# Kernel tuning notes

Measured on AMD Instinct MI355X. Metric: run time of the kernel, lower is better.

The kernel has to match this reference:

```python
import jax, jax.numpy as jnp
import numpy as np

B, N, DIM, HEADS = 4, 1024, 1024, 16
DH = DIM // HEADS
SCALE = 1.0 / np.sqrt(DH)
EPS = 1e-6


def clinear(x, Wr, Wi, br, bi):
    # (a+bi)(Wr+Wi i): real = a Wr^T - b Wi^T, imag = a Wi^T + b Wr^T
    xr, xi = x.real, x.imag
    real = xr @ Wr.T - xi @ Wi.T + br
    imag = xr @ Wi.T + xi @ Wr.T + bi
    return jax.lax.complex(real, imag)


def cln(x, gamma, beta):
    # normalize magnitude over last dim, keep phase
    mag = jnp.abs(x)
    phase = jnp.angle(x)
    mean = jnp.mean(mag, axis=-1, keepdims=True)
    var = jnp.var(mag, axis=-1, keepdims=True)
    nm = (mag - mean) / jnp.sqrt(var + EPS)
    nm = nm * gamma + beta
    return jax.lax.complex(nm * jnp.cos(phase), nm * jnp.sin(phase))


def forward(xr, xi, Wq_r, Wq_i, bq_r, bq_i, Wk_r, Wk_i, bk_r, bk_i,
            Wv_r, Wv_i, bv_r, bv_i, Wo_r, Wo_i, bo_r, bo_i,
            gq, beq, gk, bek, gv, bev):
    x = jax.lax.complex(xr, xi)  # [B,N,D] complex64

    def heads(t):
        return t.reshape(B, N, HEADS, DH).transpose(0, 2, 1, 3)  # [B,H,N,dh]

    Q = heads(cln(clinear(x, Wq_r, Wq_i, bq_r, bq_i), gq, beq))
    K = heads(cln(clinear(x, Wk_r, Wk_i, bk_r, bk_i), gk, bek))
    V = heads(cln(clinear(x, Wv_r, Wv_i, bv_r, bv_i), gv, bev))

    Qf = jnp.fft.fft(Q, axis=2, norm='ortho')
    Kf = jnp.fft.fft(K, axis=2, norm='ortho')
    Vf = jnp.fft.fft(V, axis=2, norm='ortho')

    scores = jnp.einsum('bhnd,bhmd->bhnm', Qf, jnp.conj(Kf)) * SCALE
    attn = jax.nn.softmax(scores.real, axis=-1)  # real-valued softmax
    # attn is real; multiply into complex Vf componentwise
    out_f = jax.lax.complex(jnp.einsum('bhnm,bhmd->bhnd', attn, Vf.real),
                            jnp.einsum('bhnm,bhmd->bhnd', attn, Vf.imag))
    out = jnp.fft.ifft(out_f, axis=2, norm='ortho')
    out = out.transpose(0, 2, 1, 3).reshape(B, N, DIM)
    y = clinear(out, Wo_r, Wo_i, bo_r, bo_i)
    # return real||imag concatenated on last axis (float32 view of complex output)
    return jnp.concatenate([y.real, y.imag], axis=-1)


def setup_inputs() -> dict:
    key = jax.random.key(0)
    ks = jax.random.split(key, 16)
    wscale = np.sqrt(2.0 / (DIM + DIM)).astype(np.float32)
    d = {}
    d['xr'] = jax.random.normal(ks[0], (B, N, DIM), jnp.float32)
    d['xi'] = jax.random.normal(ks[1], (B, N, DIM), jnp.float32)
    i = 2
    for name in ('q', 'k', 'v', 'o'):
        d[f'W{name}_r'] = jax.random.normal(ks[i], (DIM, DIM), jnp.float32) * wscale; i += 1
        d[f'W{name}_i'] = jax.random.normal(ks[i], (DIM, DIM), jnp.float32) * wscale; i += 1
        d[f'b{name}_r'] = jnp.zeros((DIM,), jnp.float32)
        d[f'b{name}_i'] = jnp.zeros((DIM,), jnp.float32)
    for name in ('q', 'k', 'v'):
        d[f'g{name}'] = jnp.ones((DIM,), jnp.float32)
        d[f'be{name}'] = jnp.zeros((DIM,), jnp.float32)
    return d


def reference(xr, xi, Wq_r, Wq_i, bq_r, bq_i, Wk_r, Wk_i, bk_r, bk_i,
              Wv_r, Wv_i, bv_r, bv_i, Wo_r, Wo_i, bo_r, bo_i,
              gq, beq, gk, bek, gv, bev):
    return forward(xr, xi, Wq_r, Wq_i, bq_r, bq_i, Wk_r, Wk_i, bk_r, bk_i,
                   Wv_r, Wv_i, bv_r, bv_i, Wo_r, Wo_i, bo_r, bo_i,
                   gq, beq, gk, bek, gv, bev)
```

## Files before the change

### kernel.cpp

```cpp
#include <hip/hip_runtime.h>
#include <math.h>

#define BB 4
#define NN 1024
#define DIMM 1024
#define HHH 16
#define DHH 64
#define BN 4096
#define EPS_LN 1e-6f

typedef __bf16 bf16_t;
typedef __bf16 bf16x8 __attribute__((ext_vector_type(8)));
typedef float f32x4 __attribute__((ext_vector_type(4)));
typedef float f32x16 __attribute__((ext_vector_type(16)));
#define MFMA16(a, b, c) __builtin_amdgcn_mfma_f32_16x16x32_bf16(a, b, c, 0, 0, 0)
#define MFMA32(a, b, c) __builtin_amdgcn_mfma_f32_32x32x16_bf16(a, b, c, 0, 0, 0)
#define AS1 __attribute__((address_space(1)))
#define AS3 __attribute__((address_space(3)))

__device__ inline unsigned pk2(float a, float b) {
  union { bf16_t h[2]; unsigned u; } c;
  c.h[0] = (bf16_t)a; c.h[1] = (bf16_t)b;
  return c.u;
}
union U16 { uint4 u; bf16x8 v; };

__global__ __launch_bounds__(256) void pack_x(
    const float* __restrict__ xr, const float* __restrict__ xi,
    bf16_t* __restrict__ out)
{
  int t = blockIdx.x * 256 + threadIdx.x;
  size_t e = (size_t)t * 8;
  int row = (int)(e >> 11), col = (int)(e & 2047);
  const float* src = (col < 1024) ? (xr + (size_t)row * 1024 + col)
                                  : (xi + (size_t)row * 1024 + col - 1024);
  float4 a = *(const float4*)src;
  float4 b = *(const float4*)(src + 4);
  bf16x8 o;
  o[0] = (bf16_t)a.x; o[1] = (bf16_t)a.y; o[2] = (bf16_t)a.z; o[3] = (bf16_t)a.w;
  o[4] = (bf16_t)b.x; o[5] = (bf16_t)b.y; o[6] = (bf16_t)b.z; o[7] = (bf16_t)b.w;
  *(bf16x8*)(out + e) = o;
}

__global__ __launch_bounds__(256) void pack_w(
    const float* __restrict__ Wr, const float* __restrict__ Wi,
    const float* __restrict__ br, const float* __restrict__ bi,
    bf16_t* __restrict__ Wcat, float* __restrict__ bcat)
{
  int t = blockIdx.x * 256 + threadIdx.x;
  size_t e = (size_t)t * 8;
  int row = (int)(e >> 11), col = (int)(e & 2047);
  const float* src;
  float sgn = 1.f;
  if (row < 1024) {
    if (col < 1024) src = Wr + (size_t)row * 1024 + col;
    else          { src = Wi + (size_t)row * 1024 + col - 1024; sgn = -1.f; }
  } else {
    int r2 = row - 1024;
    if (col < 1024) src = Wi + (size_t)r2 * 1024 + col;
    else            src = Wr + (size_t)r2 * 1024 + col - 1024;
  }
  float4 a = *(const float4*)src;
  float4 b = *(const float4*)(src + 4);
  bf16x8 o;
  o[0] = (bf16_t)(sgn * a.x); o[1] = (bf16_t)(sgn * a.y);
  o[2] = (bf16_t)(sgn * a.z); o[3] = (bf16_t)(sgn * a.w);
  o[4] = (bf16_t)(sgn * b.x); o[5] = (bf16_t)(sgn * b.y);
  o[6] = (bf16_t)(sgn * b.z); o[7] = (bf16_t)(sgn * b.w);
  *(bf16x8*)(Wcat + e) = o;
  if (e < 2048) {
#pragma unroll
    for (int j = 0; j < 8; ++j) {
      int n = (int)e + j;
      bcat[n] = (n < 1024) ? br[n] : bi[n - 1024];
    }
  }
}

__global__ __launch_bounds__(256) void gemm_bf16(
    const bf16_t* __restrict__ A, const bf16_t* __restrict__ Bt,
    const float* __restrict__ bias,
    float* __restrict__ Cr, float* __restrict__ Ci, int ldc)
{
  __shared__ bf16_t sA[128 * 64];
  __shared__ bf16_t sB[128 * 64];
  const int tid = threadIdx.x;
  const int w = tid >> 6, l = tid & 63;
  const int lo4 = l & 15, hi = l >> 4;
  const int wr = w >> 1, wc = w & 1;
  const int row0 = blockIdx.y * 128, col0 = blockIdx.x * 128;

  const int srow = (l >> 3);
  const int scol = (l & 7) * 8;
  const bf16_t* gA[4];
  const bf16_t* gB[4];
#pragma unroll
  for (int i = 0; i < 4; ++i) {
    int r = (w * 4 + i) * 8 + srow;
    gA[i] = A  + (size_t)(row0 + r) * 2048 + scol;
    gB[i] = Bt + (size_t)(col0 + r) * 2048 + scol;
  }

  f32x4 acc[4][4] = {};
  for (int k0 = 0; k0 < 2048; k0 += 64) {
    __syncthreads();
#pragma unroll
    for (int i = 0; i < 4; ++i) {
      __builtin_amdgcn_global_load_lds((const AS1 void*)(gA[i] + k0),
                                       (AS3 void*)&sA[(w * 4 + i) * 512], 16, 0, 0);
      __builtin_amdgcn_global_load_lds((const AS1 void*)(gB[i] + k0),
                                       (AS3 void*)&sB[(w * 4 + i) * 512], 16, 0, 0);
    }
    __syncthreads();
#pragma unroll
    for (int kk = 0; kk < 2; ++kk) {
      bf16x8 am[4], bn[4];
#pragma unroll
      for (int i = 0; i < 4; ++i)
        am[i] = *(const bf16x8*)&sA[(wr * 64 + i * 16 + lo4) * 64 + kk * 32 + hi * 8];
#pragma unroll
      for (int j = 0; j < 4; ++j)
        bn[j] = *(const bf16x8*)&sB[(wc * 64 + j * 16 + lo4) * 64 + kk * 32 + hi * 8];
#pragma unroll
      for (int i = 0; i < 4; ++i)
#pragma unroll
        for (int j = 0; j < 4; ++j)
          acc[i][j] = MFMA16(am[i], bn[j], acc[i][j]);
    }
  }
  const int colg0 = col0 + wc * 64;
  float* Cp = (colg0 < 1024) ? Cr : Ci;
  const int cb = colg0 & 1023;
#pragma unroll
  for (int i = 0; i < 4; ++i) {
#pragma unroll
    for (int j = 0; j < 4; ++j) {
      float bv = bias[colg0 + j * 16 + lo4];
#pragma unroll
      for (int r = 0; r < 4; ++r) {
        int rowg = row0 + wr * 64 + i * 16 + hi * 4 + r;
        Cp[(size_t)rowg * ldc + cb + j * 16 + lo4] = acc[i][j][r] + bv;
      }
    }
  }
}

__global__ __launch_bounds__(256) void ln_stats(
    const float* __restrict__ re, const float* __restrict__ im,
    float2* __restrict__ st)
{
  __shared__ float red[8];
  const int row = blockIdx.x;
  const int tid = threadIdx.x;
  const float* pr = re + (size_t)row * DIMM;
  const float* pi = im + (size_t)row * DIMM;
  float s = 0.f, s2 = 0.f;
#pragma unroll
  for (int t = 0; t < 4; ++t) {
    int c = tid + t * 256;
    float vr = pr[c], vi = pi[c];
    float mg = sqrtf(vr * vr + vi * vi);
    s += mg; s2 += mg * mg;
  }
#pragma unroll
  for (int o = 32; o; o >>= 1) { s += __shfl_down(s, o); s2 += __shfl_down(s2, o); }
  if ((tid & 63) == 0) { red[tid >> 6] = s; red[4 + (tid >> 6)] = s2; }
  __syncthreads();
  if (tid == 0) {
    float S = red[0] + red[1] + red[2] + red[3];
    float S2 = red[4] + red[5] + red[6] + red[7];
    float mean = S * (1.f / DIMM);
    float var = S2 * (1.f / DIMM) - mean * mean;
    st[row] = make_float2(mean, rsqrtf(var + EPS_LN));
  }
}

#define LIDX(d_, c_) ((d_) * 1025 + ((c_) ^ (((c_) >> 5) & 31)))

__global__ __launch_bounds__(512) void fft_kernel(
    const float* __restrict__ inR, const float* __restrict__ inI,
    bf16_t* __restrict__ outR, bf16_t* __restrict__ outI,
    int in_sb, int in_sh, int in_sn, int in_sd,
    int out_sb, int out_sh, int out_sn,
    float sign, float oscale, int imode, int omode,
    const float2* __restrict__ stats,
    const float* __restrict__ gamma, const float* __restrict__ beta)
{
  __shared__ float lr[16 * 1025], li[16 * 1025];
  __shared__ float2 tw[512];
  const int tid = threadIdx.x;
  const int dc = blockIdx.x & 3;
  const int bh = blockIdx.x >> 2;
  const int b = bh >> 4, h = bh & 15;
  const float* bR = inR + (size_t)b * in_sb + (size_t)h * in_sh;
  const float* bI = inI + (size_t)b * in_sb + (size_t)h * in_sh;
  {
    float ang = sign * 3.14159265358979323846f * (float)tid * (1.f / 512.f);
    float sn, cs;
    __sincosf(ang, &sn, &cs);
    tw[tid] = make_float2(cs, sn);
  }
  if (imode == 0) {
    float gg[16], bb[16];
    if (stats) {
#pragma unroll
      for (int ds = 0; ds < 16; ++ds) {
        gg[ds] = gamma[h * DHH + dc * 16 + ds];
        bb[ds] = beta[h * DHH + dc * 16 + ds];
      }
    }
#pragma unroll
    for (int rep = 0; rep < 2; ++rep) {
      int n = tid + rep * 512;
      const float* pR = bR + (size_t)n * in_sn + dc * 16;
      const float* pI = bI + (size_t)n * in_sn + dc * 16;
      union { float4 q[4]; float f[16]; } ur, ui;
#pragma unroll
      for (int k = 0; k < 4; ++k) {
        ur.q[k] = *(const float4*)(pR + k * 4);
        ui.q[k] = *(const float4*)(pI + k * 4);
      }
      if (stats) {
        float2 stv = stats[b * NN + n];
#pragma unroll
        for (int ds = 0; ds < 16; ++ds) {
          float a = ur.f[ds], c2 = ui.f[ds];
          float mag = sqrtf(a * a + c2 * c2);
          float nm = (mag - stv.x) * stv.y * gg[ds] + bb[ds];
          if (mag > 0.f) { float sc = nm / mag; ur.f[ds] = a * sc; ui.f[ds] = c2 * sc; }
          else           { ur.f[ds] = nm; ui.f[ds] = 0.f; }
        }
      }
#pragma unroll
      for (int ds = 0; ds < 16; ++ds) {
        int ax = LIDX(ds, n);
        lr[ax] = ur.f[ds];
        li[ax] = ui.f[ds];
      }
    }
  } else {
    const int ds = tid & 15, nb = tid >> 4;
    const float* pR = bR + (size_t)(dc * 16 + ds) * in_sd + nb * 32;
    const float* pI = bI + (size_t)(dc * 16 + ds) * in_sd + nb * 32;
#pragma unroll
    for (int k = 0; k < 32; k += 4) {
      float4 v = *(const float4*)(pR + k);
      float4 w = *(const float4*)(pI + k);
      int c = nb * 32 + k;
      lr[LIDX(ds, c + 0)] = v.x;  li[LIDX(ds, c + 0)] = w.x;
      lr[LIDX(ds, c + 1)] = v.y;  li[LIDX(ds, c + 1)] = w.y;
      lr[LIDX(ds, c + 2)] = v.z;  li[LIDX(ds, c + 2)] = w.z;
      lr[LIDX(ds, c + 3)] = v.w;  li[LIDX(ds, c + 3)] = w.w;
    }
  }
  __syncthreads();
  const int dsub = tid & 15;
  const int jb = tid >> 4;
  for (int hs = 9; hs >= 0; --hs) {
    int half = 1 << hs;
    for (int it = 0; it < 16; ++it) {
      int j = jb + it * 32;
      int o = j & (half - 1);
      int i0 = ((j >> hs) << (hs + 1)) + o;
      int i1 = i0 + half;
      int a0 = LIDX(dsub, i0), a1 = LIDX(dsub, i1);
      float ar = lr[a0], ai = li[a0];
      float br_ = lr[a1], bi_ = li[a1];
      lr[a0] = ar + br_;
      li[a0] = ai + bi_;
      float sr = ar - br_, si = ai - bi_;
      float2 t = tw[o << (9 - hs)];
      lr[a1] = sr * t.x - si * t.y;
      li[a1] = sr * t.y + si * t.x;
    }
    __syncthreads();
  }
  bf16_t* oRb = outR + (size_t)b * out_sb + (size_t)h * out_sh;
  bf16_t* oIb = outI + (size_t)b * out_sb + (size_t)h * out_sh;
#pragma unroll
  for (int rep = 0; rep < 2; ++rep) {
    int n = tid + rep * 512;
    int rv = __brev((unsigned)n) >> 22;
    int phi = rv ^ ((rv >> 5) & 31);
    float fr[16], fi[16];
#pragma unroll
    for (int ds = 0; ds < 16; ++ds) {
      fr[ds] = lr[ds * 1025 + phi] * oscale;
      fi[ds] = li[ds * 1025 + phi] * oscale;
    }
    if (omode == 1) {
      size_t tb = (size_t)(n >> 5) * 4096;
#pragma unroll
      for (int ds = 0; ds < 16; ++ds) {
        int dch = dc * 16 + ds;
        size_t ga = tb + (size_t)dch * 32 + ((n & 31) ^ (((dch >> 1) & 3) << 3));
        oRb[ga] = (bf16_t)fr[ds];
        oIb[ga] = (bf16_t)fi[ds];
      }
    } else {
      int cb = dc * 16, sw = 0;
      if (omode == 2) { cb = (dc ^ ((n >> 1) & 3)) * 16; sw = (n & 1) << 3; }
      bf16x8 v0, v1, w0, w1;
#pragma unroll
      for (int k = 0; k < 8; ++k) {
        v0[k] = (bf16_t)fr[k ^ sw];
        v1[k] = (bf16_t)fr[(k + 8) ^ sw];
        w0[k] = (bf16_t)fi[k ^ sw];
        w1[k] = (bf16_t)fi[(k + 8) ^ sw];
      }
      size_t gb = (size_t)n * out_sn + cb;
      *(bf16x8*)(oRb + gb) = v0;
      *(bf16x8*)(oRb + gb + 8) = v1;
      *(bf16x8*)(oIb + gb) = w0;
      *(bf16x8*)(oIb + gb + 8) = w1;
    }
  }
}

__global__ __launch_bounds__(256, 2) void fattn(
    const bf16_t* __restrict__ Qf, const bf16_t* __restrict__ Kfs,
    const bf16_t* __restrict__ Vfs, float* __restrict__ OT)
{
  __shared__ bf16_t K2[2][4096];
  __shared__ bf16_t V2[2][4096];
  const int tid = threadIdx.x;
  const int w = tid >> 6, l = tid & 63;
  const int lq = l & 31;
  const int h = l >> 5;
  const int i = blockIdx.x;
  const int j = i >> 3;
  const int bh = (i & 7) * 8 + (j >> 3);
  const int q0 = (j & 7) * 128 + w * 32;

  bf16x8 bq[8];
  const bf16_t* qp = Qf + ((size_t)bh * NN + q0 + lq) * 128 + h * 8;
#pragma unroll
  for (int kk = 0; kk < 8; ++kk) bq[kk] = *(const bf16x8*)(qp + kk * 16);

  f32x16 o[4] = {};
  float m = -3e38f, ln = 0.f;

  const bf16_t* kg = Kfs + (size_t)bh * 131072 + w * 1024 + l * 8;
  const bf16_t* vg = Vfs + (size_t)bh * 131072 + w * 1024 + l * 8;
  const int kswz = (lq & 7) << 3;
  const int vswz = ((lq >> 1) & 3) << 3;

#pragma unroll
  for (int ii = 0; ii < 2; ++ii) {
    __builtin_amdgcn_global_load_lds((const AS1 void*)(kg + ii * 512),
                                     (AS3 void*)&K2[0][w * 1024 + ii * 512], 16, 0, 0);
    __builtin_amdgcn_global_load_lds((const AS1 void*)(vg + ii * 512),
                                     (AS3 void*)&V2[0][w * 1024 + ii * 512], 16, 0, 0);
  }
  __syncthreads();

  int cur = 0;
  for (int t = 0; t < 32; ++t) {
    if (t < 31) {
      const bf16_t* kt = kg + (size_t)(t + 1) * 4096;
      const bf16_t* vt = vg + (size_t)(t + 1) * 4096;
#pragma unroll
      for (int ii = 0; ii < 2; ++ii) {
        __builtin_amdgcn_global_load_lds((const AS1 void*)(kt + ii * 512),
                                         (AS3 void*)&K2[cur ^ 1][w * 1024 + ii * 512], 16, 0, 0);
        __builtin_amdgcn_global_load_lds((const AS1 void*)(vt + ii * 512),
                                         (AS3 void*)&V2[cur ^ 1][w * 1024 + ii * 512], 16, 0, 0);
      }
    }

    f32x16 s = {};
#pragma unroll
    for (int kk = 0; kk < 8; ++kk) {
      bf16x8 ak = *(const bf16x8*)&K2[cur][lq * 128 + ((kk * 16 + h * 8) ^ kswz)];
      s = MFMA32(ak, bq[kk], s);
    }

    float pmax = s[0];
#pragma unroll
    for (int r = 1; r < 16; ++r) pmax = fmaxf(pmax, s[r]);
    pmax = fmaxf(pmax, __shfl_xor(pmax, 32));
    if (!__all(pmax - m <= 8.f)) {
      float mnew = fmaxf(m, pmax);
      float alpha = __expf(m - mnew);
      m = mnew;
      ln *= alpha;
#pragma unroll
      for (int db = 0; db < 4; ++db)
#pragma unroll
        for (int r = 0; r < 16; ++r) o[db][r] *= alpha;
    }
    float pf[16];
    float rs = 0.f;
#pragma unroll
    for (int r = 0; r < 16; ++r) { pf[r] = __expf(s[r] - m); rs += pf[r]; }
    rs += __shfl_xor(rs, 32);
    ln += rs;

    unsigned pw[8];
#pragma unroll
    for (int ii = 0; ii < 8; ++ii) pw[ii] = pk2(pf[2 * ii], pf[2 * ii + 1]);
    unsigned r0 = (unsigned)__shfl_xor((int)(h ? pw[0] : pw[2]), 32);
    unsigned r1 = (unsigned)__shfl_xor((int)(h ? pw[1] : pw[3]), 32);
    unsigned r2 = (unsigned)__shfl_xor((int)(h ? pw[4] : pw[6]), 32);
    unsigned r3 = (unsigned)__shfl_xor((int)(h ? pw[5] : pw[7]), 32);
    U16 bp0, bp1;
    bp0.u.x = h ? r0 : pw[0];  bp0.u.y = h ? r1 : pw[1];
    bp0.u.z = h ? pw[2] : r0;  bp0.u.w = h ? pw[3] : r1;
    bp1.u.x = h ? r2 : pw[4];  bp1.u.y = h ? r3 : pw[5];
    bp1.u.z = h ? pw[6] : r2;  bp1.u.w = h ? pw[7] : r3;

#pragma unroll
    for (int db = 0; db < 4; ++db) {
      int r = db * 32 + lq;
      bf16x8 av0 = *(const bf16x8*)&V2[cur][r * 32 + ((h * 8) ^ vswz)];
      bf16x8 av1 = *(const bf16x8*)&V2[cur][r * 32 + ((16 + h * 8) ^ vswz)];
      o[db] = MFMA32(av0, bp0.v, o[db]);
      o[db] = MFMA32(av1, bp1.v, o[db]);
    }

    __syncthreads();
    cur ^= 1;
  }

  float inv = 1.f / ln;
  const size_t otb = (size_t)bh * 128 * NN + q0 + lq;
#pragma unroll
  for (int db = 0; db < 4; ++db)
#pragma unroll
    for (int r = 0; r < 16; ++r) {
      int dl = (r & 3) + 8 * (r >> 2) + 4 * h;
      OT[otb + (size_t)(db * 32 + dl) * NN] = o[db][r] * inv;
    }
}

extern "C" void kernel_launch(void* const* d_in, const int* in_sizes, int n_in,
                              void* d_out, int out_size, void* d_ws, size_t ws_size,
                              hipStream_t stream) {
  const float* xr   = (const float*)d_in[0];
  const float* xi   = (const float*)d_in[1];
  const float* Wqr  = (const float*)d_in[2];
  const float* Wqi  = (const float*)d_in[3];
  const float* bqr  = (const float*)d_in[4];
  const float* bqi  = (const float*)d_in[5];
  const float* Wkr  = (const float*)d_in[6];
  const float* Wki  = (const float*)d_in[7];
  const float* bkr  = (const float*)d_in[8];
  const float* bki  = (const float*)d_in[9];
  const float* Wvr  = (const float*)d_in[10];
  const float* Wvi  = (const float*)d_in[11];
  const float* bvr  = (const float*)d_in[12];
  const float* bvi  = (const float*)d_in[13];
  const float* Wor  = (const float*)d_in[14];
  const float* Woi  = (const float*)d_in[15];
  const float* bor  = (const float*)d_in[16];
  const float* boi  = (const float*)d_in[17];
  const float* gq   = (const float*)d_in[18];
  const float* beq  = (const float*)d_in[19];
  const float* gk   = (const float*)d_in[20];
  const float* bek  = (const float*)d_in[21];
  const float* gv   = (const float*)d_in[22];
  const float* bev  = (const float*)d_in[23];

  char* wp = (char*)d_ws;
  bf16_t* Axaug = (bf16_t*)wp;  wp += (size_t)4096 * 2048 * 2;
  bf16_t* Wcat  = (bf16_t*)wp;  wp += (size_t)2048 * 2048 * 2;
  float*  bcat  = (float*)wp;   wp += (size_t)2048 * 4;
  float2* lnst  = (float2*)wp;  wp += (size_t)4096 * 8;
  float*  Ar    = (float*)wp;   wp += (size_t)4096 * 1024 * 4;
  float*  Ai    = (float*)wp;   wp += (size_t)4096 * 1024 * 4;
  bf16_t* Qf    = (bf16_t*)wp;  wp += (size_t)64 * 1024 * 128 * 2;
  bf16_t* Kf    = (bf16_t*)wp;  wp += (size_t)64 * 1024 * 128 * 2;
  bf16_t* VfT   = (bf16_t*)wp;  wp += (size_t)64 * 1024 * 128 * 2;
  bf16_t* Yaug  = Qf;
  float*  OT    = Ar;

  const dim3 gGemm(16, 32);
  const int gPackX = (4096 * 2048 / 8) / 256;
  const int gPackW = (2048 * 2048 / 8) / 256;
  const int gFft = 64 * 4;
  const int gAtt = 64 * 8;

  pack_x<<<gPackX, 256, 0, stream>>>(xr, xi, Axaug);

  pack_w<<<gPackW, 256, 0, stream>>>(Wqr, Wqi, bqr, bqi, Wcat, bcat);
  gemm_bf16<<<gGemm, 256, 0, stream>>>(Axaug, Wcat, bcat, Ar, Ai, 1024);
  ln_stats<<<BN, 256, 0, stream>>>(Ar, Ai, lnst);
  fft_kernel<<<gFft, 512, 0, stream>>>(Ar, Ai, Qf, Qf + 64,
      NN * DIMM, DHH, DIMM, 1,
      16 * NN * 128, NN * 128, 128,
      -1.0f, 0.03125f * 0.125f, 0, 0, lnst, gq, beq);
  pack_w<<<gPackW, 256, 0, stream>>>(Wkr, Wki, bkr, bki, Wcat, bcat);
  gemm_bf16<<<gGemm, 256, 0, stream>>>(Axaug, Wcat, bcat, Ar, Ai, 1024);
  ln_stats<<<BN, 256, 0, stream>>>(Ar, Ai, lnst);
  fft_kernel<<<gFft, 512, 0, stream>>>(Ar, Ai, Kf, Kf + 64,
      NN * DIMM, DHH, DIMM, 1,
      16 * NN * 128, NN * 128, 128,
      -1.0f, 0.03125f, 0, 2, lnst, gk, bek);
  pack_w<<<gPackW, 256, 0, stream>>>(Wvr, Wvi, bvr, bvi, Wcat, bcat);
  gemm_bf16<<<gGemm, 256, 0, stream>>>(Axaug, Wcat, bcat, Ar, Ai, 1024);
  ln_stats<<<BN, 256, 0, stream>>>(Ar, Ai, lnst);
  fft_kernel<<<gFft, 512, 0, stream>>>(Ar, Ai, VfT, VfT + 2048,
      NN * DIMM, DHH, DIMM, 1,
      16 * 131072, 131072, 0,
      -1.0f, 0.03125f, 0, 1, lnst, gv, bev);
  fattn<<<gAtt, 256, 0, stream>>>(Qf, Kf, VfT, OT);
  fft_kernel<<<gFft, 512, 0, stream>>>(OT, OT + (size_t)64 * NN, Yaug, Yaug + 1024,
      16 * 128 * NN, 128 * NN, 1, NN,
      NN * 2048, 64, 2048,
      +1.0f, 0.03125f, 1, 0, nullptr, nullptr, nullptr);
  float* yout = (float*)d_out;
  pack_w<<<gPackW, 256, 0, stream>>>(Wor, Woi, bor, boi, Wcat, bcat);
  gemm_bf16<<<gGemm, 256, 0, stream>>>(Yaug, Wcat, bcat, yout, yout + 1024, 2048);
}
```

Baseline: 476.5 us.

## Switch shared-memory FFT to radix-4 with eight columns per block

The FFT kernel now uses radix-4 butterflies, so it runs 5 passes and 5 block barriers instead of 10 radix-2 passes. Each block handles 8 head-dim columns instead of 16, which halves shared-memory use and doubles the grid to 512 blocks. The padded shared-memory layout is replaced by an XOR swizzle, and the output reads use a digit-reversed index. The omode 2 output swizzle is rewritten for 8-column chunks, and its column permutation is equivalent to the old one, so the unchanged attention kernel still reads Kf correctly.

```diff
diff --git a/kernel.cpp b/kernel.cpp
--- a/kernel.cpp
+++ b/kernel.cpp
@@ -175,7 +175,7 @@
   }
 }
 
-#define LIDX(d_, c_) ((d_) * 1025 + ((c_) ^ (((c_) >> 5) & 31)))
+#define LIDX(d_, c_) (((d_) << 10) + ((c_) ^ (((c_) >> 5) & 31) ^ (((d_) & 7) << 2)))
 
 __global__ __launch_bounds__(512) void fft_kernel(
     const float* __restrict__ inR, const float* __restrict__ inI,
@@ -186,44 +186,42 @@
     const float2* __restrict__ stats,
     const float* __restrict__ gamma, const float* __restrict__ beta)
 {
-  __shared__ float lr[16 * 1025], li[16 * 1025];
-  __shared__ float2 tw[512];
+  __shared__ float lr[8 * 1024], li[8 * 1024];
+  __shared__ float2 tw[1024];
   const int tid = threadIdx.x;
-  const int dc = blockIdx.x & 3;
-  const int bh = blockIdx.x >> 2;
+  const int dc = blockIdx.x & 7;
+  const int bh = blockIdx.x >> 3;
   const int b = bh >> 4, h = bh & 15;
   const float* bR = inR + (size_t)b * in_sb + (size_t)h * in_sh;
   const float* bI = inI + (size_t)b * in_sb + (size_t)h * in_sh;
-  {
-    float ang = sign * 3.14159265358979323846f * (float)tid * (1.f / 512.f);
+#pragma unroll
+  for (int t = tid; t < 1024; t += 512) {
+    float ang = sign * 3.14159265358979323846f * (float)t * (1.f / 512.f);
     float sn, cs;
     __sincosf(ang, &sn, &cs);
-    tw[tid] = make_float2(cs, sn);
+    tw[t] = make_float2(cs, sn);
   }
   if (imode == 0) {
-    float gg[16], bb[16];
+    float gg[8], bb[8];
     if (stats) {
 #pragma unroll
-      for (int ds = 0; ds < 16; ++ds) {
-        gg[ds] = gamma[h * DHH + dc * 16 + ds];
-        bb[ds] = beta[h * DHH + dc * 16 + ds];
+      for (int ds = 0; ds < 8; ++ds) {
+        gg[ds] = gamma[h * DHH + dc * 8 + ds];
+        bb[ds] = beta[h * DHH + dc * 8 + ds];
       }
     }
 #pragma unroll
     for (int rep = 0; rep < 2; ++rep) {
       int n = tid + rep * 512;
-      const float* pR = bR + (size_t)n * in_sn + dc * 16;
-      const float* pI = bI + (size_t)n * in_sn + dc * 16;
-      union { float4 q[4]; float f[16]; } ur, ui;
-#pragma unroll
-      for (int k = 0; k < 4; ++k) {
-        ur.q[k] = *(const float4*)(pR + k * 4);
-        ui.q[k] = *(const float4*)(pI + k * 4);
-      }
+      const float* pR = bR + (size_t)n * in_sn + dc * 8;
+      const float* pI = bI + (size_t)n * in_sn + dc * 8;
+      union { float4 q[2]; float f[8]; } ur, ui;
+      ur.q[0] = *(const float4*)pR;      ur.q[1] = *(const float4*)(pR + 4);
+      ui.q[0] = *(const float4*)pI;      ui.q[1] = *(const float4*)(pI + 4);
       if (stats) {
         float2 stv = stats[b * NN + n];
 #pragma unroll
-        for (int ds = 0; ds < 16; ++ds) {
+        for (int ds = 0; ds < 8; ++ds) {
           float a = ur.f[ds], c2 = ui.f[ds];
           float mag = sqrtf(a * a + c2 * c2);
           float nm = (mag - stv.x) * stv.y * gg[ds] + bb[ds];
@@ -232,21 +230,21 @@
         }
       }
 #pragma unroll
-      for (int ds = 0; ds < 16; ++ds) {
+      for (int ds = 0; ds < 8; ++ds) {
         int ax = LIDX(ds, n);
         lr[ax] = ur.f[ds];
         li[ax] = ui.f[ds];
       }
     }
   } else {
-    const int ds = tid & 15, nb = tid >> 4;
-    const float* pR = bR + (size_t)(dc * 16 + ds) * in_sd + nb * 32;
-    const float* pI = bI + (size_t)(dc * 16 + ds) * in_sd + nb * 32;
-#pragma unroll
-    for (int k = 0; k < 32; k += 4) {
+    const int ds = tid & 7, nb = tid >> 3;
+    const float* pR = bR + (size_t)(dc * 8 + ds) * in_sd + nb * 16;
+    const float* pI = bI + (size_t)(dc * 8 + ds) * in_sd + nb * 16;
+#pragma unroll
+    for (int k = 0; k < 16; k += 4) {
       float4 v = *(const float4*)(pR + k);
       float4 w = *(const float4*)(pI + k);
-      int c = nb * 32 + k;
+      int c = nb * 16 + k;
       lr[LIDX(ds, c + 0)] = v.x;  li[LIDX(ds, c + 0)] = w.x;
       lr[LIDX(ds, c + 1)] = v.y;  li[LIDX(ds, c + 1)] = w.y;
       lr[LIDX(ds, c + 2)] = v.z;  li[LIDX(ds, c + 2)] = w.z;
@@ -254,65 +252,76 @@
     }
   }
   __syncthreads();
-  const int dsub = tid & 15;
-  const int jb = tid >> 4;
-  for (int hs = 9; hs >= 0; --hs) {
-    int half = 1 << hs;
-    for (int it = 0; it < 16; ++it) {
-      int j = jb + it * 32;
-      int o = j & (half - 1);
-      int i0 = ((j >> hs) << (hs + 1)) + o;
-      int i1 = i0 + half;
-      int a0 = LIDX(dsub, i0), a1 = LIDX(dsub, i1);
-      float ar = lr[a0], ai = li[a0];
-      float br_ = lr[a1], bi_ = li[a1];
-      lr[a0] = ar + br_;
-      li[a0] = ai + bi_;
-      float sr = ar - br_, si = ai - bi_;
-      float2 t = tw[o << (9 - hs)];
-      lr[a1] = sr * t.x - si * t.y;
-      li[a1] = sr * t.y + si * t.x;
+  const int dsub = tid & 7;
+  const int jb = tid >> 3;
+  int lq2 = 8;
+  for (int st = 0; st < 5; ++st) {
+    const int qtr = 1 << lq2;
+    const int tmul = 1 << (2 * st);
+    for (int jt = 0; jt < 4; ++jt) {
+      int j = jb + jt * 64;
+      int o = j & (qtr - 1);
+      int i0 = ((j >> lq2) << (lq2 + 2)) + o;
+      int a0 = LIDX(dsub, i0);
+      int a1 = LIDX(dsub, i0 + qtr);
+      int a2 = LIDX(dsub, i0 + 2 * qtr);
+      int a3 = LIDX(dsub, i0 + 3 * qtr);
+      float x0r = lr[a0], x0i = li[a0];
+      float x1r = lr[a1], x1i = li[a1];
+      float x2r = lr[a2], x2i = li[a2];
+      float x3r = lr[a3], x3i = li[a3];
+      float ar = x0r + x2r, ai2 = x0i + x2i;
+      float br = x0r - x2r, bi  = x0i - x2i;
+      float cr = x1r + x3r, ci  = x1i + x3i;
+      float dr = x1r - x3r, di  = x1i - x3i;
+      float2 t1 = tw[o * tmul];
+      float2 t2 = tw[2 * o * tmul];
+      float2 t3 = tw[3 * o * tmul];
+      lr[a0] = ar + cr;  li[a0] = ai2 + ci;
+      float u1r = br - sign * di, u1i = bi + sign * dr;
+      lr[a1] = u1r * t1.x - u1i * t1.y;  li[a1] = u1r * t1.y + u1i * t1.x;
+      float u2r = ar - cr, u2i = ai2 - ci;
+      lr[a2] = u2r * t2.x - u2i * t2.y;  li[a2] = u2r * t2.y + u2i * t2.x;
+      float u3r = br + sign * di, u3i = bi - sign * dr;
+      lr[a3] = u3r * t3.x - u3i * t3.y;  li[a3] = u3r * t3.y + u3i * t3.x;
     }
     __syncthreads();
+    lq2 -= 2;
   }
   bf16_t* oRb = outR + (size_t)b * out_sb + (size_t)h * out_sh;
   bf16_t* oIb = outI + (size_t)b * out_sb + (size_t)h * out_sh;
 #pragma unroll
   for (int rep = 0; rep < 2; ++rep) {
     int n = tid + rep * 512;
-    int rv = __brev((unsigned)n) >> 22;
-    int phi = rv ^ ((rv >> 5) & 31);
-    float fr[16], fi[16];
-#pragma unroll
-    for (int ds = 0; ds < 16; ++ds) {
-      fr[ds] = lr[ds * 1025 + phi] * oscale;
-      fi[ds] = li[ds * 1025 + phi] * oscale;
+    int rv2 = __brev((unsigned)n) >> 22;
+    int p = ((rv2 & 0x155) << 1) | ((rv2 >> 1) & 0x155);
+    float fr[8], fi[8];
+#pragma unroll
+    for (int ds = 0; ds < 8; ++ds) {
+      fr[ds] = lr[LIDX(ds, p)] * oscale;
+      fi[ds] = li[LIDX(ds, p)] * oscale;
     }
     if (omode == 1) {
       size_t tb = (size_t)(n >> 5) * 4096;
 #pragma unroll
-      for (int ds = 0; ds < 16; ++ds) {
-        int dch = dc * 16 + ds;
+      for (int ds = 0; ds < 8; ++ds) {
+        int dch = dc * 8 + ds;
         size_t ga = tb + (size_t)dch * 32 + ((n & 31) ^ (((dch >> 1) & 3) << 3));
         oRb[ga] = (bf16_t)fr[ds];
         oIb[ga] = (bf16_t)fi[ds];
       }
     } else {
-      int cb = dc * 16, sw = 0;
-      if (omode == 2) { cb = (dc ^ ((n >> 1) & 3)) * 16; sw = (n & 1) << 3; }
-      bf16x8 v0, v1, w0, w1;
+      int cb = dc * 8;
+      if (omode == 2) cb = (dc ^ (n & 7)) * 8;
+      bf16x8 v0, w0;
 #pragma unroll
       for (int k = 0; k < 8; ++k) {
-        v0[k] = (bf16_t)fr[k ^ sw];
-        v1[k] = (bf16_t)fr[(k + 8) ^ sw];
-        w0[k] = (bf16_t)fi[k ^ sw];
-        w1[k] = (bf16_t)fi[(k + 8) ^ sw];
+        v0[k] = (bf16_t)fr[k];
+        w0[k] = (bf16_t)fi[k];
       }
       size_t gb = (size_t)n * out_sn + cb;
       *(bf16x8*)(oRb + gb) = v0;
-      *(bf16x8*)(oRb + gb + 8) = v1;
       *(bf16x8*)(oIb + gb) = w0;
-      *(bf16x8*)(oIb + gb + 8) = w1;
     }
   }
 }
@@ -477,7 +486,7 @@
   const dim3 gGemm(16, 32);
   const int gPackX = (4096 * 2048 / 8) / 256;
   const int gPackW = (2048 * 2048 / 8) / 256;
-  const int gFft = 64 * 4;
+  const int gFft = 64 * 8;
   const int gAtt = 64 * 8;
 
   pack_x<<<gPackX, 256, 0, stream>>>(xr, xi, Axaug);
```

Result: faster. 431.7 us (-9.4%).
